# Optimization experiments

Measured on AMD Instinct MI355X. Metric: run time of the kernel, lower is better.

Reference implementation:

```python
import jax, jax.numpy as jnp
import numpy as np

D_MODEL = 256; N_LEVELS = 4; N_HEADS = 8; N_POINTS = 4
H_SP = 32; W_SP = 32
B = 2; LEN_Q = 1024; LEN_IN = N_LEVELS * H_SP * W_SP
D_HEAD = D_MODEL // N_HEADS
K9 = 9 * N_POINTS  # 3x3 neighborhood around each of the top-k matches


def setup_inputs() -> dict:
    key = jax.random.key(0)
    k1, k2, k3, k4 = jax.random.split(key, 4)
    bound = (6.0 / (D_MODEL + D_MODEL)) ** 0.5  # xavier_uniform for output_proj
    return {
        "query": jax.random.normal(k1, (B, LEN_Q, D_MODEL), jnp.float32),
        "reference_points": jax.random.uniform(k2, (B, LEN_Q, N_LEVELS, 2), dtype=jnp.float32),
        "input_flatten": jax.random.normal(k3, (B, LEN_IN, D_MODEL), jnp.float32),
        # all levels share the same h==w==32 spatial shape (required by the module)
        "input_spatial_shapes": np.full((N_LEVELS, 2), H_SP, dtype=np.int64),
        "input_level_start_index": (np.arange(N_LEVELS) * H_SP * W_SP).astype(np.int64),
        "out_proj_w": jax.random.uniform(k4, (D_MODEL, D_MODEL), jnp.float32, -bound, bound),
        "out_proj_b": jnp.zeros((D_MODEL,), jnp.float32),
    }


def _sample_offset(query, input_flatten, h, w, t):
    # per-head correlation -> softmax -> top-k index -> 3x3 neighborhood -> (x,y) offsets
    n, lq, _ = query.shape
    q = query.reshape(n, lq, N_HEADS, D_HEAD)
    v = input_flatten.reshape(n, -1, N_HEADS, D_HEAD)
    corr = jnp.einsum('nqhd,nkhd->nhqk', q, v) / D_HEAD          # [n,H,lq,Lin]
    corr = corr.reshape(n, N_HEADS, lq, t, h * w)
    prob = jax.nn.softmax(10.0 * corr, axis=-1)
    _, idx = jax.lax.top_k(prob, N_POINTS)                        # [n,H,lq,t,P] int32
    deltas = jnp.array([-1 - h, -h, 1 - h, -1, 0, 1, -1 + h, h, 1 + h], jnp.int32)
    # torch cat order is delta-major: all P points for delta1, then delta2, ...
    res = (idx[..., None, :] + deltas[:, None]).reshape(n, N_HEADS, lq, t, K9)
    res = jnp.clip(res, 0, (h - 1) * (w - 1))                     # faithful (h-1)*(w-1) clamp
    resf = res.astype(jnp.float32)
    off_w = jnp.floor(resf / h)
    off_h = resf - off_w * h
    offsets = jnp.stack([off_w, off_h], axis=-1)                  # [n,H,lq,t,K9,2]
    return jnp.transpose(offsets, (0, 2, 1, 3, 4, 5))             # [n,lq,H,L,K9,2]


def _ms_deform_attn(value, loc, h, w):
    # value [n,Lin,H,dh]; loc in [0,1], [n,lq,H,L,K9,2]; grid_sample-style bilinear, zero pad
    n, lq = loc.shape[0], loc.shape[1]
    v = value.reshape(n, N_LEVELS, h * w, N_HEADS, D_HEAD)
    v = jnp.transpose(v, (0, 3, 1, 2, 4))                         # [n,H,L,hw,dh]
    x = loc[..., 0] * w - 0.5
    y = loc[..., 1] * h - 0.5
    x0 = jnp.floor(x); y0 = jnp.floor(y)
    lw = x - x0; lh = y - y0
    attn_w = 1.0 / (N_LEVELS * K9)  # softmax of all-ones buffer is uniform
    acc = jnp.zeros((n, lq, N_HEADS, D_HEAD), jnp.float32)
    corners = ((y0, x0, (1 - lh) * (1 - lw)), (y0, x0 + 1, (1 - lh) * lw),
               (y0 + 1, x0, lh * (1 - lw)), (y0 + 1, x0 + 1, lh * lw))
    for yi, xi, wgt in corners:
        valid = (yi >= 0) & (yi < h) & (xi >= 0) & (xi < w)
        ii = (jnp.clip(yi, 0, h - 1) * w + jnp.clip(xi, 0, w - 1)).astype(jnp.int32)
        ww = jnp.where(valid, wgt, 0.0) * attn_w                  # [n,lq,H,L,K9]
        ii_t = jnp.transpose(ii, (0, 2, 3, 1, 4)).reshape(n, N_HEADS, N_LEVELS, lq * K9)
        g = jnp.take_along_axis(v, ii_t[..., None], axis=3)       # [n,H,L,lq*K9,dh]
        g = g.reshape(n, N_HEADS, N_LEVELS, lq, K9, D_HEAD)
        ww_t = jnp.transpose(ww, (0, 2, 3, 1, 4))                 # [n,H,L,lq,K9]
        acc = acc + jnp.einsum('nhlqk,nhlqkd->nqhd', ww_t, g)
    return acc.reshape(n, lq, D_MODEL)


def reference(query, reference_points, input_flatten, input_spatial_shapes,
              input_level_start_index, out_proj_w, out_proj_b):
    ss = np.asarray(input_spatial_shapes)
    h = int(ss[0, 0]); w = h
    lin = input_flatten.shape[1]
    t = lin // (h * w)  # == N_LEVELS
    value = input_flatten.reshape(input_flatten.shape[0], lin, N_HEADS, D_HEAD)
    offsets = _sample_offset(query, input_flatten, h, w, t)
    assert reference_points.shape[-1] == 2
    normalizer = jnp.asarray(np.stack([ss[:, 1], ss[:, 0]], -1), jnp.float32)  # [L,2]=(w,h)
    loc = offsets / normalizer[None, None, None, :, None, :]
    out = _ms_deform_attn(value, loc, h, w)
    out = out @ out_proj_w.T + out_proj_b
    return out, loc
```

## Files before the change

kernel.cpp:

```cpp
#include <hip/hip_runtime.h>
#include <math.h>

#define BB 2
#define LQ 1024
#define DM 256
#define NH 8
#define DH 32
#define NL 4
#define HWsp 1024
#define LIN 4096
#define K9 36

typedef short bf16x8 __attribute__((ext_vector_type(8)));
typedef float f32x4 __attribute__((ext_vector_type(4)));

__device__ __forceinline__ ushort bf16rn(float x) {
  unsigned u = __float_as_uint(x);
  unsigned r = (u + 0x7FFFu + ((u >> 16) & 1u)) >> 16;
  return (ushort)r;
}
__device__ __forceinline__ float bf16tof(ushort h) {
  return __uint_as_float(((unsigned)h) << 16);
}

#define INSERT4(val, index)                                              \
  {                                                                      \
    const float v_ = (val);                                              \
    const int ix_ = (index);                                             \
    if (v_ > v3) {                                                       \
      if (v_ > v1) {                                                     \
        if (v_ > v0) {                                                   \
          v3 = v2; i3 = i2; v2 = v1; i2 = i1; v1 = v0; i1 = i0;          \
          v0 = v_; i0 = ix_;                                             \
        } else {                                                         \
          v3 = v2; i3 = i2; v2 = v1; i2 = i1; v1 = v_; i1 = ix_;         \
        }                                                                \
      } else {                                                           \
        if (v_ > v2) {                                                   \
          v3 = v2; i3 = i2; v2 = v_; i2 = ix_;                           \
        } else {                                                         \
          v3 = v_; i3 = ix_;                                             \
        }                                                                \
      }                                                                  \
    }                                                                    \
  }

#define LMAX(av, ai, bv, bi)                                        \
  {                                                                 \
    const bool g_ = ((av) > (bv)) || ((av) == (bv) && (ai) < (bi)); \
    if (!g_) { (av) = (bv); (ai) = (bi); }                          \
  }
#define CEX(av, ai, bv, bi)                                         \
  {                                                                 \
    const bool g_ = ((av) > (bv)) || ((av) == (bv) && (ai) < (bi)); \
    const float tv_ = g_ ? (av) : (bv);                             \
    const int ti_ = g_ ? (ai) : (bi);                               \
    (bv) = g_ ? (bv) : (av); (bi) = g_ ? (bi) : (ai);               \
    (av) = tv_; (ai) = ti_;                                         \
  }

#define PSTRIDE ((size_t)BB * NL * NH * 1024 * 32)

__global__ __launch_bounds__(256) void vsplit_kernel(
    const float* __restrict__ value, ushort* __restrict__ vs) {
  const int T = blockIdx.x * 256 + threadIdx.x;
  const int flat = T << 3;
  const int n = flat >> 20;
  const int rem = flat & 0xFFFFF;
  const int lin = rem >> 8;
  const int d0 = rem & 255;
  const int l = lin >> 10, row = lin & 1023;
  const int h = d0 >> 5, dd = d0 & 31;

  const float* src = value + (size_t)flat;
  float xf[8];
  *(float4*)&xf[0] = *(const float4*)src;
  *(float4*)&xf[4] = *(const float4*)(src + 4);

  ushort uh[8], ul[8], ul2[8];
  #pragma unroll
  for (int j = 0; j < 8; ++j) {
    const float x = xf[j];
    const ushort h1 = bf16rn(x);
    const float r1 = x - bf16tof(h1);
    const ushort h2 = bf16rn(r1);
    const float r2 = r1 - bf16tof(h2);
    uh[j] = h1; ul[j] = h2; ul2[j] = bf16rn(r2);
  }
  const size_t ob =
      ((((size_t)((n * NL + l) * NH + h)) << 10) + row) * 32 + dd;
  *(bf16x8*)(vs + 0 * PSTRIDE + ob) =
      (bf16x8){(short)uh[0], (short)uh[1], (short)uh[2], (short)uh[3],
               (short)uh[4], (short)uh[5], (short)uh[6], (short)uh[7]};
  *(bf16x8*)(vs + 1 * PSTRIDE + ob) =
      (bf16x8){(short)ul[0], (short)ul[1], (short)ul[2], (short)ul[3],
               (short)ul[4], (short)ul[5], (short)ul[6], (short)ul[7]};
  *(bf16x8*)(vs + 2 * PSTRIDE + ob) =
      (bf16x8){(short)ul2[0], (short)ul2[1], (short)ul2[2], (short)ul2[3],
               (short)ul2[4], (short)ul2[5], (short)ul2[6], (short)ul2[7]};
}

template <int PRESPLIT>
__global__ __launch_bounds__(256) void corr_topk_kernel(
    const float* __restrict__ query, const float* __restrict__ value,
    const ushort* __restrict__ vs, int* __restrict__ idx_out) {
  __shared__ ushort hiL[128][40];
  __shared__ ushort loL[128][40];
  __shared__ ushort lo2L[128][40];

  const int tid = threadIdx.x;
  const int nh = blockIdx.z;
  const int n = nh >> 3, h = nh & 7;
  const int l = blockIdx.y;
  const int w = tid >> 6, L = tid & 63;
  const int qtile = (blockIdx.x << 2) + w;
  const int r16 = L & 15, g = L >> 4;

  bf16x8 qhi, qlo, qlo2;
  {
    const float* qp =
        query + (size_t)(n * LQ + (qtile << 4) + r16) * DM + h * DH + (g << 3);
    float qf[8];
    *(float4*)&qf[0] = *(const float4*)qp;
    *(float4*)&qf[4] = *(const float4*)(qp + 4);
    ushort uh[8], ul[8], ul2[8];
    #pragma unroll
    for (int j = 0; j < 8; ++j) {
      const float x = qf[j];
      const ushort h1 = bf16rn(x);
      const float r1 = x - bf16tof(h1);
      const ushort h2 = bf16rn(r1);
      const float r2 = r1 - bf16tof(h2);
      uh[j] = h1; ul[j] = h2; ul2[j] = bf16rn(r2);
    }
    qhi = (bf16x8){(short)uh[0], (short)uh[1], (short)uh[2], (short)uh[3],
                   (short)uh[4], (short)uh[5], (short)uh[6], (short)uh[7]};
    qlo = (bf16x8){(short)ul[0], (short)ul[1], (short)ul[2], (short)ul[3],
                   (short)ul[4], (short)ul[5], (short)ul[6], (short)ul[7]};
    qlo2 = (bf16x8){(short)ul2[0], (short)ul2[1], (short)ul2[2], (short)ul2[3],
                    (short)ul2[4], (short)ul2[5], (short)ul2[6], (short)ul2[7]};
  }

  float v0 = -INFINITY, v1 = -INFINITY, v2 = -INFINITY, v3 = -INFINITY;
  int i0 = 0, i1 = 0, i2 = 0, i3 = 0;

  const float* vbase = value + (size_t)(n * LIN + l * HWsp) * DM + h * DH;
  const ushort* psbase =
      vs + ((((size_t)((n * NL + l) * NH + h)) << 10)) * 32;
  const int srow = tid >> 1, scol = (tid & 1) << 4;

  for (int c = 0; c < 8; ++c) {
    if (PRESPLIT) {
      const size_t off = ((size_t)(c << 7)) * 32 + ((size_t)tid << 4);
      const ushort* s_hi = psbase + off;
      const ushort* s_lo = psbase + PSTRIDE + off;
      const ushort* s_lo2 = psbase + 2 * PSTRIDE + off;
      *(bf16x8*)&hiL[srow][scol] = *(const bf16x8*)s_hi;
      *(bf16x8*)&hiL[srow][scol + 8] = *(const bf16x8*)(s_hi + 8);
      *(bf16x8*)&loL[srow][scol] = *(const bf16x8*)s_lo;
      *(bf16x8*)&loL[srow][scol + 8] = *(const bf16x8*)(s_lo + 8);
      *(bf16x8*)&lo2L[srow][scol] = *(const bf16x8*)s_lo2;
      *(bf16x8*)&lo2L[srow][scol + 8] = *(const bf16x8*)(s_lo2 + 8);
    } else {
      const float* vp = vbase + (size_t)((c << 7) + srow) * DM + scol;
      float xf[16];
      *(float4*)&xf[0] = *(const float4*)vp;
      *(float4*)&xf[4] = *(const float4*)(vp + 4);
      *(float4*)&xf[8] = *(const float4*)(vp + 8);
      *(float4*)&xf[12] = *(const float4*)(vp + 12);
      ushort uh[16], ul[16], ul2[16];
      #pragma unroll
      for (int j = 0; j < 16; ++j) {
        const float x = xf[j];
        const ushort h1 = bf16rn(x);
        const float r1 = x - bf16tof(h1);
        const ushort h2 = bf16rn(r1);
        const float r2 = r1 - bf16tof(h2);
        uh[j] = h1; ul[j] = h2; ul2[j] = bf16rn(r2);
      }
      #pragma unroll
      for (int hv = 0; hv < 2; ++hv) {
        const int o = hv << 3;
        *(bf16x8*)&hiL[srow][scol + o] =
            (bf16x8){(short)uh[o], (short)uh[o + 1], (short)uh[o + 2], (short)uh[o + 3],
                     (short)uh[o + 4], (short)uh[o + 5], (short)uh[o + 6], (short)uh[o + 7]};
        *(bf16x8*)&loL[srow][scol + o] =
            (bf16x8){(short)ul[o], (short)ul[o + 1], (short)ul[o + 2], (short)ul[o + 3],
                     (short)ul[o + 4], (short)ul[o + 5], (short)ul[o + 6], (short)ul[o + 7]};
        *(bf16x8*)&lo2L[srow][scol + o] =
            (bf16x8){(short)ul2[o], (short)ul2[o + 1], (short)ul2[o + 2], (short)ul2[o + 3],
                     (short)ul2[o + 4], (short)ul2[o + 5], (short)ul2[o + 6], (short)ul2[o + 7]};
      }
    }
    __syncthreads();

    #pragma unroll
    for (int t = 0; t < 8; ++t) {
      const int row = (t << 4) + r16;
      const bf16x8 ahi = *(const bf16x8*)&hiL[row][g << 3];
      const bf16x8 alo = *(const bf16x8*)&loL[row][g << 3];
      const bf16x8 alo2 = *(const bf16x8*)&lo2L[row][g << 3];
      f32x4 acc = {0.f, 0.f, 0.f, 0.f};
      acc = __builtin_amdgcn_mfma_f32_16x16x32_bf16(alo2, qhi, acc, 0, 0, 0);
      acc = __builtin_amdgcn_mfma_f32_16x16x32_bf16(ahi, qlo2, acc, 0, 0, 0);
      acc = __builtin_amdgcn_mfma_f32_16x16x32_bf16(alo, qlo, acc, 0, 0, 0);
      acc = __builtin_amdgcn_mfma_f32_16x16x32_bf16(alo, qhi, acc, 0, 0, 0);
      acc = __builtin_amdgcn_mfma_f32_16x16x32_bf16(ahi, qlo, acc, 0, 0, 0);
      acc = __builtin_amdgcn_mfma_f32_16x16x32_bf16(ahi, qhi, acc, 0, 0, 0);
      const int kb = (c << 7) + (t << 4) + (g << 2);
      INSERT4(acc[0], kb + 0);
      INSERT4(acc[1], kb + 1);
      INSERT4(acc[2], kb + 2);
      INSERT4(acc[3], kb + 3);
    }
    __syncthreads();
  }

  #pragma unroll
  for (int m = 16; m < 64; m <<= 1) {
    const float b0 = __shfl_xor(v0, m);
    const float b1 = __shfl_xor(v1, m);
    const float b2 = __shfl_xor(v2, m);
    const float b3 = __shfl_xor(v3, m);
    const int j0 = __shfl_xor(i0, m);
    const int j1 = __shfl_xor(i1, m);
    const int j2 = __shfl_xor(i2, m);
    const int j3 = __shfl_xor(i3, m);
    LMAX(v0, i0, b3, j3);
    LMAX(v1, i1, b2, j2);
    LMAX(v2, i2, b1, j1);
    LMAX(v3, i3, b0, j0);
    CEX(v0, i0, v2, i2);
    CEX(v1, i1, v3, i3);
    CEX(v0, i0, v1, i1);
    CEX(v2, i2, v3, i3);
  }

  if (L < 16) {
    const int q = (qtile << 4) + L;
    ((int4*)idx_out)[(((size_t)nh * NL + l) << 10) + q] = make_int4(i0, i1, i2, i3);
  }
}

__global__ __launch_bounds__(256) void loc_kernel(const int* __restrict__ idx_buf,
                                                  float* __restrict__ loc) {
  const int t = blockIdx.x * 256 + threadIdx.x;
  const int k = t % 36;
  int rest = t / 36;
  const int l = rest & 3; rest >>= 2;
  const int h = rest & 7; rest >>= 3;
  const int q = rest & 1023;
  const int n = rest >> 10;
  const int p = k & 3, dd = k >> 2;
  const int idx = idx_buf[(((((n << 3) + h) * NL + l) << 10) + q) * 4 + p];
  const int delta = ((dd / 3) - 1) * 32 + (dd % 3) - 1;
  int res = idx + delta;
  res = min(max(res, 0), 961);
  const int W = res >> 5, H = res & 31;
  ((float2*)loc)[t] = make_float2((float)W * 0.03125f, (float)H * 0.03125f);
}

__global__ __launch_bounds__(256) void gather_kernel(
    const float* __restrict__ value, const int* __restrict__ idx_buf,
    float* __restrict__ acc_out) {
  __shared__ float red[NL][DM];
  const int nq = blockIdx.x;
  const int n = nq >> 10, q = nq & 1023;
  const int tid = threadIdx.x;
  const int l = tid >> 6;
  const int h = (tid >> 3) & 7;
  const int d4 = tid & 7;

  const int4 id4 =
      ((const int4*)idx_buf)[((((size_t)((n << 3) + h)) * NL + l) << 10) + q];

  const float4* vb4 =
      (const float4*)(value + (size_t)(n * LIN + l * HWsp) * DM + h * DH) + d4;

  float4 a = make_float4(0.f, 0.f, 0.f, 0.f);
  #pragma unroll
  for (int p = 0; p < 4; ++p) {
    const int idx = (p == 0) ? id4.x : (p == 1) ? id4.y : (p == 2) ? id4.z : id4.w;
    #pragma unroll
    for (int dy = -1; dy <= 1; ++dy) {
      #pragma unroll
      for (int dx = -1; dx <= 1; ++dx) {
        int res = idx + dy * 32 + dx;
        res = min(max(res, 0), 961);
        const int W = res >> 5, H = res & 31;
        const int g = (H << 5) + W;
        const float wW = (W >= 1) ? 1.f : 0.f;
        const float wH = (H >= 1) ? 1.f : 0.f;
        const float wB = wW * wH;
        const float4 c0 = vb4[(size_t)g * 64];
        const float4 c1 = vb4[(size_t)max(g - 1, 0) * 64];
        const float4 c2 = vb4[(size_t)max(g - 32, 0) * 64];
        const float4 c3 = vb4[(size_t)max(g - 33, 0) * 64];
        a.x += c0.x + wW * c1.x + wH * c2.x + wB * c3.x;
        a.y += c0.y + wW * c1.y + wH * c2.y + wB * c3.y;
        a.z += c0.z + wW * c1.z + wH * c2.z + wB * c3.z;
        a.w += c0.w + wW * c1.w + wH * c2.w + wB * c3.w;
      }
    }
  }

  const int col = h * DH + d4 * 4;
  red[l][col + 0] = a.x;
  red[l][col + 1] = a.y;
  red[l][col + 2] = a.z;
  red[l][col + 3] = a.w;
  __syncthreads();
  const float s = red[0][tid] + red[1][tid] + red[2][tid] + red[3][tid];
  acc_out[(size_t)nq * DM + tid] = s * (1.0f / 576.0f);
}

__global__ __launch_bounds__(256) void proj_kernel(
    const float* __restrict__ acc_in, const float* __restrict__ W,
    const float* __restrict__ bias, float* __restrict__ out) {
  __shared__ float la[8][256];
  const int qb = blockIdx.x << 3;
  const int tid = threadIdx.x;
  for (int i = tid; i < 8 * 256; i += 256)
    la[i >> 8][i & 255] = acc_in[((size_t)qb << 8) + i];
  __syncthreads();
  const float* wrow = W + (size_t)tid * 256;
  float s0 = 0.f, s1 = 0.f, s2 = 0.f, s3 = 0.f, s4 = 0.f, s5 = 0.f, s6 = 0.f, s7 = 0.f;
  for (int c0 = 0; c0 < 256; c0 += 4) {
    const float4 wv = *(const float4*)(wrow + c0);
    #define PROJ_STEP(qi, sreg)                                   \
      {                                                           \
        const float4 av = *(const float4*)&la[qi][c0];            \
        sreg = fmaf(wv.x, av.x, sreg);                            \
        sreg = fmaf(wv.y, av.y, sreg);                            \
        sreg = fmaf(wv.z, av.z, sreg);                            \
        sreg = fmaf(wv.w, av.w, sreg);                            \
      }
    PROJ_STEP(0, s0) PROJ_STEP(1, s1) PROJ_STEP(2, s2) PROJ_STEP(3, s3)
    PROJ_STEP(4, s4) PROJ_STEP(5, s5) PROJ_STEP(6, s6) PROJ_STEP(7, s7)
    #undef PROJ_STEP
  }
  const float bj = bias[tid];
  out[(size_t)(qb + 0) * 256 + tid] = s0 + bj;
  out[(size_t)(qb + 1) * 256 + tid] = s1 + bj;
  out[(size_t)(qb + 2) * 256 + tid] = s2 + bj;
  out[(size_t)(qb + 3) * 256 + tid] = s3 + bj;
  out[(size_t)(qb + 4) * 256 + tid] = s4 + bj;
  out[(size_t)(qb + 5) * 256 + tid] = s5 + bj;
  out[(size_t)(qb + 6) * 256 + tid] = s6 + bj;
  out[(size_t)(qb + 7) * 256 + tid] = s7 + bj;
}

extern "C" void kernel_launch(void* const* d_in, const int* in_sizes, int n_in,
                              void* d_out, int out_size, void* d_ws, size_t ws_size,
                              hipStream_t stream) {
  (void)in_sizes; (void)n_in; (void)out_size;
  const float* query = (const float*)d_in[0];
  const float* value = (const float*)d_in[2];
  const float* opw = (const float*)d_in[5];
  const float* opb = (const float*)d_in[6];

  float* out = (float*)d_out;
  float* loc = out + (size_t)BB * LQ * DM;

  const size_t SPLITB = 3 * PSTRIDE * sizeof(ushort);
  const size_t IDXB = (size_t)BB * NH * NL * LQ * 4 * sizeof(int);
  const size_t ACCB = (size_t)BB * LQ * DM * sizeof(float);

  if (ws_size >= SPLITB + IDXB + ACCB) {
    ushort* vs = (ushort*)d_ws;
    int* idx_buf = (int*)((char*)d_ws + SPLITB);
    float* acc_buf = (float*)((char*)d_ws + SPLITB + IDXB);

    vsplit_kernel<<<dim3(1024), 256, 0, stream>>>(value, vs);
    corr_topk_kernel<1><<<dim3(16, NL, BB * NH), 256, 0, stream>>>(
        query, value, vs, idx_buf);
    loc_kernel<<<dim3((BB * LQ * NH * NL * K9) / 256), 256, 0, stream>>>(idx_buf, loc);
    gather_kernel<<<dim3(BB * LQ), 256, 0, stream>>>(value, idx_buf, acc_buf);
    proj_kernel<<<dim3(BB * LQ / 8), 256, 0, stream>>>(acc_buf, opw, opb, out);
  } else {
    int* idx_buf = (int*)d_ws;
    float* acc_buf = (float*)((char*)d_ws + IDXB);

    corr_topk_kernel<0><<<dim3(16, NL, BB * NH), 256, 0, stream>>>(
        query, value, (const ushort*)nullptr, idx_buf);
    loc_kernel<<<dim3((BB * LQ * NH * NL * K9) / 256), 256, 0, stream>>>(idx_buf, loc);
    gather_kernel<<<dim3(BB * LQ), 256, 0, stream>>>(value, idx_buf, acc_buf);
    proj_kernel<<<dim3(BB * LQ / 8), 256, 0, stream>>>(acc_buf, opw, opb, out);
  }
}
```

Measured before the change: 120.3 us.

## Split top-k key range across blocks, merge partials, and restructure gather per head

The correlation/top-k kernel now splits the key range in two halves across separate blocks, doubling the grid. A new merge kernel combines the two partial top-4 lists, and LDS tiles shrink to 64 rows with an XOR swizzle to avoid bank conflicts. The gather kernel is relaunched per (query, head) with 256 threads. Interior points use a factored 2-load weighted sum instead of 36 bilinear loads, with a shuffle-based reduction. This adds parallelism and cuts gather loads, at the cost of an extra launch and partial-result traffic.

```diff
diff --git a/kernel.cpp b/kernel.cpp
--- a/kernel.cpp
+++ b/kernel.cpp
@@ -10,6 +10,7 @@
 #define HWsp 1024
 #define LIN 4096
 #define K9 36
+#define NGRP (BB * NH * NL * LQ)
 
 typedef short bf16x8 __attribute__((ext_vector_type(8)));
 typedef float f32x4 __attribute__((ext_vector_type(4)));
@@ -87,8 +88,7 @@
     const float r2 = r1 - bf16tof(h2);
     uh[j] = h1; ul[j] = h2; ul2[j] = bf16rn(r2);
   }
-  const size_t ob =
-      ((((size_t)((n * NL + l) * NH + h)) << 10) + row) * 32 + dd;
+  const size_t ob = ((((size_t)((n * NL + l) * NH + h)) << 10) + row) * 32 + dd;
   *(bf16x8*)(vs + 0 * PSTRIDE + ob) =
       (bf16x8){(short)uh[0], (short)uh[1], (short)uh[2], (short)uh[3],
                (short)uh[4], (short)uh[5], (short)uh[6], (short)uh[7]};
@@ -100,20 +100,25 @@
                (short)ul2[4], (short)ul2[5], (short)ul2[6], (short)ul2[7]};
 }
 
-template <int PRESPLIT>
+template <int SPLIT, int PRESPLIT>
 __global__ __launch_bounds__(256) void corr_topk_kernel(
     const float* __restrict__ query, const float* __restrict__ value,
-    const ushort* __restrict__ vs, int* __restrict__ idx_out) {
-  __shared__ ushort hiL[128][40];
-  __shared__ ushort loL[128][40];
-  __shared__ ushort lo2L[128][40];
+    const ushort* __restrict__ vs, int* __restrict__ idx_out,
+    float4* __restrict__ pval, int4* __restrict__ pidx) {
+  __shared__ ushort hiL[64][40];
+  __shared__ ushort loL[64][40];
+  __shared__ ushort lo2L[64][40];
 
   const int tid = threadIdx.x;
   const int nh = blockIdx.z;
   const int n = nh >> 3, h = nh & 7;
   const int l = blockIdx.y;
+  const int qc = (SPLIT == 2) ? ((int)blockIdx.x >> 1) : (int)blockIdx.x;
+  const int half = (SPLIT == 2) ? ((int)blockIdx.x & 1) : 0;
+  const int c0 = (SPLIT == 2) ? (half << 3) : 0;
+  const int c1 = (SPLIT == 2) ? (c0 + 8) : 16;
   const int w = tid >> 6, L = tid & 63;
-  const int qtile = (blockIdx.x << 2) + w;
+  const int qtile = (qc << 2) + w;
   const int r16 = L & 15, g = L >> 4;
 
   bf16x8 qhi, qlo, qlo2;
@@ -144,33 +149,26 @@
   float v0 = -INFINITY, v1 = -INFINITY, v2 = -INFINITY, v3 = -INFINITY;
   int i0 = 0, i1 = 0, i2 = 0, i3 = 0;
 
+  const int srow = tid >> 2, s = tid & 3;
+  const int wslot = (s ^ (srow & 3)) << 3;
+  const ushort* psbase =
+      PRESPLIT ? vs + ((((size_t)((n * NL + l) * NH + h)) << 10)) * 32 : nullptr;
   const float* vbase = value + (size_t)(n * LIN + l * HWsp) * DM + h * DH;
-  const ushort* psbase =
-      vs + ((((size_t)((n * NL + l) * NH + h)) << 10)) * 32;
-  const int srow = tid >> 1, scol = (tid & 1) << 4;
-
-  for (int c = 0; c < 8; ++c) {
+
+  for (int c = c0; c < c1; ++c) {
     if (PRESPLIT) {
-      const size_t off = ((size_t)(c << 7)) * 32 + ((size_t)tid << 4);
-      const ushort* s_hi = psbase + off;
-      const ushort* s_lo = psbase + PSTRIDE + off;
-      const ushort* s_lo2 = psbase + 2 * PSTRIDE + off;
-      *(bf16x8*)&hiL[srow][scol] = *(const bf16x8*)s_hi;
-      *(bf16x8*)&hiL[srow][scol + 8] = *(const bf16x8*)(s_hi + 8);
-      *(bf16x8*)&loL[srow][scol] = *(const bf16x8*)s_lo;
-      *(bf16x8*)&loL[srow][scol + 8] = *(const bf16x8*)(s_lo + 8);
-      *(bf16x8*)&lo2L[srow][scol] = *(const bf16x8*)s_lo2;
-      *(bf16x8*)&lo2L[srow][scol + 8] = *(const bf16x8*)(s_lo2 + 8);
+      const size_t off = ((size_t)((c << 6) + srow)) * 32 + (s << 3);
+      *(bf16x8*)&hiL[srow][wslot] = *(const bf16x8*)(psbase + off);
+      *(bf16x8*)&loL[srow][wslot] = *(const bf16x8*)(psbase + PSTRIDE + off);
+      *(bf16x8*)&lo2L[srow][wslot] = *(const bf16x8*)(psbase + 2 * PSTRIDE + off);
     } else {
-      const float* vp = vbase + (size_t)((c << 7) + srow) * DM + scol;
-      float xf[16];
+      const float* vp = vbase + (size_t)((c << 6) + srow) * DM + (s << 3);
+      float xf[8];
       *(float4*)&xf[0] = *(const float4*)vp;
       *(float4*)&xf[4] = *(const float4*)(vp + 4);
-      *(float4*)&xf[8] = *(const float4*)(vp + 8);
-      *(float4*)&xf[12] = *(const float4*)(vp + 12);
-      ushort uh[16], ul[16], ul2[16];
+      ushort uh[8], ul[8], ul2[8];
       #pragma unroll
-      for (int j = 0; j < 16; ++j) {
+      for (int j = 0; j < 8; ++j) {
         const float x = xf[j];
         const ushort h1 = bf16rn(x);
         const float r1 = x - bf16tof(h1);
@@ -178,28 +176,25 @@
         const float r2 = r1 - bf16tof(h2);
         uh[j] = h1; ul[j] = h2; ul2[j] = bf16rn(r2);
       }
-      #pragma unroll
-      for (int hv = 0; hv < 2; ++hv) {
-        const int o = hv << 3;
-        *(bf16x8*)&hiL[srow][scol + o] =
-            (bf16x8){(short)uh[o], (short)uh[o + 1], (short)uh[o + 2], (short)uh[o + 3],
-                     (short)uh[o + 4], (short)uh[o + 5], (short)uh[o + 6], (short)uh[o + 7]};
-        *(bf16x8*)&loL[srow][scol + o] =
-            (bf16x8){(short)ul[o], (short)ul[o + 1], (short)ul[o + 2], (short)ul[o + 3],
-                     (short)ul[o + 4], (short)ul[o + 5], (short)ul[o + 6], (short)ul[o + 7]};
-        *(bf16x8*)&lo2L[srow][scol + o] =
-            (bf16x8){(short)ul2[o], (short)ul2[o + 1], (short)ul2[o + 2], (short)ul2[o + 3],
-                     (short)ul2[o + 4], (short)ul2[o + 5], (short)ul2[o + 6], (short)ul2[o + 7]};
-      }
+      *(bf16x8*)&hiL[srow][wslot] =
+          (bf16x8){(short)uh[0], (short)uh[1], (short)uh[2], (short)uh[3],
+                   (short)uh[4], (short)uh[5], (short)uh[6], (short)uh[7]};
+      *(bf16x8*)&loL[srow][wslot] =
+          (bf16x8){(short)ul[0], (short)ul[1], (short)ul[2], (short)ul[3],
+                   (short)ul[4], (short)ul[5], (short)ul[6], (short)ul[7]};
+      *(bf16x8*)&lo2L[srow][wslot] =
+          (bf16x8){(short)ul2[0], (short)ul2[1], (short)ul2[2], (short)ul2[3],
+                   (short)ul2[4], (short)ul2[5], (short)ul2[6], (short)ul2[7]};
     }
     __syncthreads();
 
     #pragma unroll
-    for (int t = 0; t < 8; ++t) {
+    for (int t = 0; t < 4; ++t) {
       const int row = (t << 4) + r16;
-      const bf16x8 ahi = *(const bf16x8*)&hiL[row][g << 3];
-      const bf16x8 alo = *(const bf16x8*)&loL[row][g << 3];
-      const bf16x8 alo2 = *(const bf16x8*)&lo2L[row][g << 3];
+      const int rslot = (g ^ (row & 3)) << 3;
+      const bf16x8 ahi = *(const bf16x8*)&hiL[row][rslot];
+      const bf16x8 alo = *(const bf16x8*)&loL[row][rslot];
+      const bf16x8 alo2 = *(const bf16x8*)&lo2L[row][rslot];
       f32x4 acc = {0.f, 0.f, 0.f, 0.f};
       acc = __builtin_amdgcn_mfma_f32_16x16x32_bf16(alo2, qhi, acc, 0, 0, 0);
       acc = __builtin_amdgcn_mfma_f32_16x16x32_bf16(ahi, qlo2, acc, 0, 0, 0);
@@ -207,7 +202,7 @@
       acc = __builtin_amdgcn_mfma_f32_16x16x32_bf16(alo, qhi, acc, 0, 0, 0);
       acc = __builtin_amdgcn_mfma_f32_16x16x32_bf16(ahi, qlo, acc, 0, 0, 0);
       acc = __builtin_amdgcn_mfma_f32_16x16x32_bf16(ahi, qhi, acc, 0, 0, 0);
-      const int kb = (c << 7) + (t << 4) + (g << 2);
+      const int kb = (c << 6) + (t << 4) + (g << 2);
       INSERT4(acc[0], kb + 0);
       INSERT4(acc[1], kb + 1);
       INSERT4(acc[2], kb + 2);
@@ -238,8 +233,35 @@
 
   if (L < 16) {
     const int q = (qtile << 4) + L;
-    ((int4*)idx_out)[(((size_t)nh * NL + l) << 10) + q] = make_int4(i0, i1, i2, i3);
-  }
+    const size_t gi = (((size_t)nh * NL + l) << 10) + q;
+    if (SPLIT == 2) {
+      pval[gi * 2 + half] = make_float4(v0, v1, v2, v3);
+      pidx[gi * 2 + half] = make_int4(i0, i1, i2, i3);
+    } else {
+      ((int4*)idx_out)[gi] = make_int4(i0, i1, i2, i3);
+    }
+  }
+}
+
+__global__ __launch_bounds__(256) void merge_topk_kernel(
+    const float4* __restrict__ pval, const int4* __restrict__ pidx,
+    int* __restrict__ idx_out) {
+  const int t = blockIdx.x * 256 + threadIdx.x;
+  const float4 av = pval[t * 2 + 0];
+  const int4 ai = pidx[t * 2 + 0];
+  const float4 bv = pval[t * 2 + 1];
+  const int4 bi = pidx[t * 2 + 1];
+  float w0 = av.x, w1 = av.y, w2 = av.z, w3 = av.w;
+  int m0 = ai.x, m1 = ai.y, m2 = ai.z, m3 = ai.w;
+  LMAX(w0, m0, bv.w, bi.w);
+  LMAX(w1, m1, bv.z, bi.z);
+  LMAX(w2, m2, bv.y, bi.y);
+  LMAX(w3, m3, bv.x, bi.x);
+  CEX(w0, m0, w2, m2);
+  CEX(w1, m1, w3, m3);
+  CEX(w0, m0, w1, m1);
+  CEX(w2, m2, w3, m3);
+  ((int4*)idx_out)[t] = make_int4(m0, m1, m2, m3);
 }
 
 __global__ __launch_bounds__(256) void loc_kernel(const int* __restrict__ idx_buf,
@@ -263,17 +285,18 @@
 __global__ __launch_bounds__(256) void gather_kernel(
     const float* __restrict__ value, const int* __restrict__ idx_buf,
     float* __restrict__ acc_out) {
-  __shared__ float red[NL][DM];
-  const int nq = blockIdx.x;
+  __shared__ float4 red[NL][8];
+  const int bh = blockIdx.x;
+  const int h = bh & 7;
+  const int nq = bh >> 3;
   const int n = nq >> 10, q = nq & 1023;
   const int tid = threadIdx.x;
   const int l = tid >> 6;
-  const int h = (tid >> 3) & 7;
-  const int d4 = tid & 7;
+  const int L = tid & 63;
+  const int cp = L >> 3, d4 = L & 7;
 
   const int4 id4 =
       ((const int4*)idx_buf)[((((size_t)((n << 3) + h)) * NL + l) << 10) + q];
-
   const float4* vb4 =
       (const float4*)(value + (size_t)(n * LIN + l * HWsp) * DM + h * DH) + d4;
 
@@ -281,37 +304,63 @@
   #pragma unroll
   for (int p = 0; p < 4; ++p) {
     const int idx = (p == 0) ? id4.x : (p == 1) ? id4.y : (p == 2) ? id4.z : id4.w;
-    #pragma unroll
-    for (int dy = -1; dy <= 1; ++dy) {
+    const int H0 = idx & 31, W0 = idx >> 5;
+    if (H0 >= 2 && H0 <= 30 && W0 >= 2 && W0 <= 28) {
+      const int idxT = (H0 << 5) + W0;
+      const int c0i = cp << 1;
+      const int ax0 = c0i & 3, ay = c0i >> 2;
+      const int r0 = idxT + (ax0 - 2) * 32 + (ay - 2);
+      const float wy = (ay == 1 || ay == 2) ? 2.f : 1.f;
+      const float f0 = ((ax0 == 2) ? 2.f : 1.f) * wy;
+      const float f1 = ((ax0 + 1 == 1) ? 2.f : 1.f) * wy;
+      const float4 va = vb4[(size_t)r0 * 64];
+      const float4 vbb = vb4[(size_t)(r0 + 32) * 64];
+      a.x += f0 * va.x + f1 * vbb.x;
+      a.y += f0 * va.y + f1 * vbb.y;
+      a.z += f0 * va.z + f1 * vbb.z;
+      a.w += f0 * va.w + f1 * vbb.w;
+    } else {
       #pragma unroll
-      for (int dx = -1; dx <= 1; ++dx) {
+      for (int it = 0; it < 5; ++it) {
+        const int u = cp + (it << 3);
+        const int cell = u >> 2, corner = u & 3;
+        const int dy = (cell >= 3) + (cell >= 6) - 1;
+        const int dx = cell - (dy + 1) * 3 - 1;
         int res = idx + dy * 32 + dx;
         res = min(max(res, 0), 961);
         const int W = res >> 5, H = res & 31;
-        const int g = (H << 5) + W;
-        const float wW = (W >= 1) ? 1.f : 0.f;
-        const float wH = (H >= 1) ? 1.f : 0.f;
-        const float wB = wW * wH;
-        const float4 c0 = vb4[(size_t)g * 64];
-        const float4 c1 = vb4[(size_t)max(g - 1, 0) * 64];
-        const float4 c2 = vb4[(size_t)max(g - 32, 0) * 64];
-        const float4 c3 = vb4[(size_t)max(g - 33, 0) * 64];
-        a.x += c0.x + wW * c1.x + wH * c2.x + wB * c3.x;
-        a.y += c0.y + wW * c1.y + wH * c2.y + wB * c3.y;
-        a.z += c0.z + wW * c1.z + wH * c2.z + wB * c3.z;
-        a.w += c0.w + wW * c1.w + wH * c2.w + wB * c3.w;
+        const int cw = corner & 1, ch = corner >> 1;
+        const bool ok = (u < 36) && (W >= cw) && (H >= ch);
+        const int row = ok ? (((H - ch) << 5) + (W - cw)) : 0;
+        const float wgt = ok ? 1.f : 0.f;
+        const float4 v = vb4[(size_t)row * 64];
+        a.x += wgt * v.x;
+        a.y += wgt * v.y;
+        a.z += wgt * v.z;
+        a.w += wgt * v.w;
       }
     }
   }
 
-  const int col = h * DH + d4 * 4;
-  red[l][col + 0] = a.x;
-  red[l][col + 1] = a.y;
-  red[l][col + 2] = a.z;
-  red[l][col + 3] = a.w;
+  #pragma unroll
+  for (int m = 8; m < 64; m <<= 1) {
+    a.x += __shfl_xor(a.x, m);
+    a.y += __shfl_xor(a.y, m);
+    a.z += __shfl_xor(a.z, m);
+    a.w += __shfl_xor(a.w, m);
+  }
+  if (L < 8) red[l][L] = a;
   __syncthreads();
-  const float s = red[0][tid] + red[1][tid] + red[2][tid] + red[3][tid];
-  acc_out[(size_t)nq * DM + tid] = s * (1.0f / 576.0f);
+  if (tid < 8) {
+    const float4 s0 = red[0][tid], s1 = red[1][tid], s2 = red[2][tid],
+                 s3 = red[3][tid];
+    float4 o;
+    o.x = (s0.x + s1.x + s2.x + s3.x) * (1.0f / 576.0f);
+    o.y = (s0.y + s1.y + s2.y + s3.y) * (1.0f / 576.0f);
+    o.z = (s0.z + s1.z + s2.z + s3.z) * (1.0f / 576.0f);
+    o.w = (s0.w + s1.w + s2.w + s3.w) * (1.0f / 576.0f);
+    ((float4*)(acc_out + (size_t)nq * DM + h * DH))[tid] = o;
+  }
 }
 
 __global__ __launch_bounds__(256) void proj_kernel(
@@ -363,28 +412,45 @@
   float* loc = out + (size_t)BB * LQ * DM;
 
   const size_t SPLITB = 3 * PSTRIDE * sizeof(ushort);
-  const size_t IDXB = (size_t)BB * NH * NL * LQ * 4 * sizeof(int);
+  const size_t PARTB = (size_t)NGRP * 2 * 16;
+  const size_t IDXB = (size_t)NGRP * 4 * sizeof(int);
   const size_t ACCB = (size_t)BB * LQ * DM * sizeof(float);
 
-  if (ws_size >= SPLITB + IDXB + ACCB) {
-    ushort* vs = (ushort*)d_ws;
-    int* idx_buf = (int*)((char*)d_ws + SPLITB);
-    float* acc_buf = (float*)((char*)d_ws + SPLITB + IDXB);
-
-    vsplit_kernel<<<dim3(1024), 256, 0, stream>>>(value, vs);
-    corr_topk_kernel<1><<<dim3(16, NL, BB * NH), 256, 0, stream>>>(
-        query, value, vs, idx_buf);
+  if (ws_size >= SPLITB + 2 * PARTB + IDXB + ACCB) {
+    ushort* vsb = (ushort*)d_ws;
+    float4* pval = (float4*)((char*)d_ws + SPLITB);
+    int4* pidx = (int4*)((char*)d_ws + SPLITB + PARTB);
+    int* idx_buf = (int*)((char*)d_ws + SPLITB + 2 * PARTB);
+    float* acc_buf = (float*)((char*)d_ws + SPLITB + 2 * PARTB + IDXB);
+
+    vsplit_kernel<<<dim3(1024), 256, 0, stream>>>(value, vsb);
+    corr_topk_kernel<2, 1><<<dim3(32, NL, BB * NH), 256, 0, stream>>>(
+        query, value, vsb, idx_buf, pval, pidx);
+    merge_topk_kernel<<<dim3(NGRP / 256), 256, 0, stream>>>(pval, pidx, idx_buf);
     loc_kernel<<<dim3((BB * LQ * NH * NL * K9) / 256), 256, 0, stream>>>(idx_buf, loc);
-    gather_kernel<<<dim3(BB * LQ), 256, 0, stream>>>(value, idx_buf, acc_buf);
+    gather_kernel<<<dim3(BB * LQ * NH), 256, 0, stream>>>(value, idx_buf, acc_buf);
+    proj_kernel<<<dim3(BB * LQ / 8), 256, 0, stream>>>(acc_buf, opw, opb, out);
+  } else if (ws_size >= 2 * PARTB + IDXB + ACCB) {
+    float4* pval = (float4*)d_ws;
+    int4* pidx = (int4*)((char*)d_ws + PARTB);
+    int* idx_buf = (int*)((char*)d_ws + 2 * PARTB);
+    float* acc_buf = (float*)((char*)d_ws + 2 * PARTB + IDXB);
+
+    corr_topk_kernel<2, 0><<<dim3(32, NL, BB * NH), 256, 0, stream>>>(
+        query, value, (const ushort*)nullptr, idx_buf, pval, pidx);
+    merge_topk_kernel<<<dim3(NGRP / 256), 256, 0, stream>>>(pval, pidx, idx_buf);
+    loc_kernel<<<dim3((BB * LQ * NH * NL * K9) / 256), 256, 0, stream>>>(idx_buf, loc);
+    gather_kernel<<<dim3(BB * LQ * NH), 256, 0, stream>>>(value, idx_buf, acc_buf);
     proj_kernel<<<dim3(BB * LQ / 8), 256, 0, stream>>>(acc_buf, opw, opb, out);
   } else {
     int* idx_buf = (int*)d_ws;
     float* acc_buf = (float*)((char*)d_ws + IDXB);
 
-    corr_topk_kernel<0><<<dim3(16, NL, BB * NH), 256, 0, stream>>>(
-        query, value, (const ushort*)nullptr, idx_buf);
+    corr_topk_kernel<1, 0><<<dim3(16, NL, BB * NH), 256, 0, stream>>>(
+        query, value, (const ushort*)nullptr, idx_buf, (float4*)nullptr,
+        (int4*)nullptr);
     loc_kernel<<<dim3((BB * LQ * NH * NL * K9) / 256), 256, 0, stream>>>(idx_buf, loc);
-    gather_kernel<<<dim3(BB * LQ), 256, 0, stream>>>(value, idx_buf, acc_buf);
+    gather_kernel<<<dim3(BB * LQ * NH), 256, 0, stream>>>(value, idx_buf, acc_buf);
     proj_kernel<<<dim3(BB * LQ / 8), 256, 0, stream>>>(acc_buf, opw, opb, out);
   }
 }
```

After: 104.4 us. 1.15x faster.
